# Optimization experiments

Hardware: AMD Instinct MI355X
Metric: run time of the kernel (lower is better)

Reference implementation:

```python
import jax, jax.numpy as jnp
import numpy as np
from jax.scipy.linalg import solve_triangular

L_SUB = 16          # subarray length (init arg L)
DL = 0.05           # diagonal loading factor


def setup_inputs() -> dict:
    key = jax.random.key(0)
    k0, k1, k2 = jax.random.split(key, 3)
    B, C, NS, NZ, NX = 2, 128, 1024, 256, 128
    rf = jax.random.normal(k0, (B, C, NS), jnp.float32)
    t0 = jnp.zeros((B,), jnp.float32)
    d_tx = jax.random.uniform(k1, (B, NZ, NX), dtype=jnp.float32)
    d_rx = jax.random.uniform(k2, (C, NZ, NX), dtype=jnp.float32)
    fs = jnp.float32((NS - 1) / 2.0)   # keeps sample positions in [0, NS-1]
    f0 = jnp.float32(5.0)              # unused by forward (kept for signature parity)
    c0 = jnp.float32(1.0)
    apod = jnp.ones((C,), jnp.float32) # unused by forward
    return dict(rf=rf, t0=t0, d_tx=d_tx, d_rx=d_rx, fs=fs, f0=f0, c0=c0, apod=apod)


def _aligned_signals(rf, t0, d_tx, d_rx, fs, c0):
    """Bilinear (1-D linear) resample of rf at per-pixel delays.
    Equivalent to torch grid_sample(mode='bilinear', padding_mode='border',
    align_corners=True) where the grid x-coord is samples*2/(NS-1)-1."""
    B, C, NS = rf.shape
    _, NZ, NX = d_tx.shape
    # samples: [B, C, NZ, NX] fractional sample index into rf
    samples = fs * ((d_tx[:, None, :, :] + d_rx[None, :, :, :]) / c0
                    + t0[:, None, None, None])
    pos = jnp.clip(samples, 0.0, NS - 1.0)          # border padding
    i0 = jnp.floor(pos).astype(jnp.int32)
    i1 = jnp.minimum(i0 + 1, NS - 1)
    frac = pos - i0.astype(pos.dtype)
    sig = rf.reshape(B * C, NS)
    i0f = i0.reshape(B * C, NZ * NX)
    i1f = i1.reshape(B * C, NZ * NX)
    v0 = jnp.take_along_axis(sig, i0f, axis=1).reshape(B, C, NZ, NX)
    v1 = jnp.take_along_axis(sig, i1f, axis=1).reshape(B, C, NZ, NX)
    return v0 * (1.0 - frac) + v1 * frac


def reference(rf, t0, d_tx, d_rx, fs, f0, c0, apod):
    B, C, NS = rf.shape
    _, NZ, NX = d_tx.shape
    M = C - L_SUB + 1  # number of subarrays (113)
    aligned = _aligned_signals(rf, t0, d_tx, d_rx, fs, c0)  # [B, C, NZ, NX]
    # per-pixel channel vectors: [P, C], P = B*NZ*NX
    xf = aligned.transpose(0, 2, 3, 1).reshape(-1, C)
    # subarray gather: S[p, m, l] = xf[p, m + l]  -> [P, M, L]
    idx = jnp.arange(M)[:, None] + jnp.arange(L_SUB)[None, :]
    S = xf[:, idx]
    # avg_pool1d(kernel=M, stride=1) over channels == mean over subarray axis
    x = S.mean(axis=1)                                  # [P, L]
    # spatially-smoothed covariance: R = S^T S / M, symmetrized
    R = jnp.einsum('pml,pmk->plk', S, S) / M
    R = 0.5 * (R + R.transpose(0, 2, 1))
    # diagonal loading: R += dl * (trace/L) * I
    delta = jnp.trace(R, axis1=-2, axis2=-1) / L_SUB    # [P]
    R = R + (DL * delta)[:, None, None] * jnp.eye(L_SUB, dtype=R.dtype)
    # Cholesky solve R u = 1
    Lc = jnp.linalg.cholesky(R)
    rhs = jnp.ones((R.shape[0], L_SUB, 1), R.dtype)
    y1 = solve_triangular(Lc, rhs, lower=True)
    u = solve_triangular(Lc, y1, lower=True, trans=1)[..., 0]  # [P, L]
    # MVDR weights (steering a = ones) and beamformed output
    denom = jnp.sum(u, axis=-1, keepdims=True) + 1e-10
    w = u / denom
    y = jnp.sum(w * x, axis=-1)                         # [P]
    return y.reshape(B, NZ, NX)
```

## Files before the change

kernel.cpp:

```cpp
#include <hip/hip_runtime.h>


namespace {

constexpr int kB  = 2;
constexpr int kC  = 128;
constexpr int kNS = 1024;
constexpr int kNZ = 256;
constexpr int kNX = 128;
constexpr int kZX = kNZ * kNX;
constexpr int kTPB = 256;

__device__ __host__ constexpr int tri(int l, int k) {
  return l * 16 - (l * (l - 1)) / 2 + (k - l);
}

template <bool HEAD>
__device__ __forceinline__ void chunk16(
    const float* __restrict__ rfq,
    const float* __restrict__ drxp, int cbase, float kk, float base,
    float (&F)[16], float (&win)[16], float (&head)[16], float& Sall) {
  float dr[16];
#pragma unroll
  for (int r = 0; r < 16; ++r) dr[r] = drxp[(size_t)(cbase + r) * kZX];

  float2 vv[16];
  float fr[16];
#pragma unroll
  for (int r = 0; r < 16; ++r) {
    float pos = fmaf(kk, dr[r], base);
    pos = fminf(fmaxf(pos, 0.0f), 1023.0f);
    int i0 = (int)pos;
    i0 = min(i0, kNS - 2);
    fr[r] = pos - (float)i0;
    __builtin_memcpy(&vv[r], rfq + r * kNS + i0, 8);
  }

#pragma unroll
  for (int r = 0; r < 16; ++r) {
    float v = fmaf(fr[r], vv[r].y - vv[r].x, vv[r].x);
    Sall += v;
    F[0] = fmaf(v, v, F[0]);
    if constexpr (HEAD) {
#pragma unroll
      for (int d = 1; d <= r; ++d) F[d] = fmaf(v, win[r - d], F[d]);
      head[r] = v;
    } else {
#pragma unroll
      for (int d = 1; d < 16; ++d) F[d] = fmaf(v, win[(r - d) & 15], F[d]);
    }
    win[r] = v;
  }
}

__global__ __launch_bounds__(kTPB, 1) void mvb_kernel(
    const float* __restrict__ rf, const float* __restrict__ t0,
    const float* __restrict__ d_tx, const float* __restrict__ d_rx,
    const float* __restrict__ fs_p, const float* __restrict__ c0_p,
    float* __restrict__ out) {
  const int tid = threadIdx.x;
  const int b = blockIdx.x >> 7;
  const int z = ((blockIdx.x & 127) << 1) + (tid >> 7);
  const int x = tid & 127;
  const int pix = (int)((size_t)b * kZX + z * kNX + x);

  const float fs = fs_p[0];
  const float c0 = c0_p[0];
  const float kk = fs / c0;
  const float base = fs * (d_tx[pix] / c0 + t0[b]);

  const float* rfb = rf + (size_t)b * kC * kNS;
  const float* drxp = d_rx + (size_t)z * kNX + x;

  float F[16], win[16], head[16];
  float Sall = 0.0f;
#pragma unroll
  for (int i = 0; i < 16; ++i) F[i] = 0.0f;

  chunk16<true>(rfb, drxp, 0, kk, base, F, win, head, Sall);
#pragma unroll 1
  for (int q = 1; q < 8; ++q)
    chunk16<false>(rfb + (size_t)q * 16 * kNS, drxp, q * 16, kk, base, F, win,
                   head, Sall);

  float Ru[136];
#pragma unroll
  for (int d = 0; d < 16; ++d) {
    float t0s = 0.0f;
#pragma unroll
    for (int i = d + 1; i < 16; ++i) t0s = fmaf(win[i - d], win[i], t0s);
    Ru[tri(0, d)] = F[d] - t0s;
#pragma unroll
    for (int l = 1; l < 16 - d; ++l)
      Ru[tri(l, l + d)] = Ru[tri(l - 1, l - 1 + d)] -
                          head[l - 1] * head[l - 1 + d] +
                          win[l] * win[l + d];
  }

  float tr = 0.0f;
#pragma unroll
  for (int l = 0; l < 16; ++l) tr += Ru[tri(l, l)];
  const float dl = tr * (0.05f / 16.0f);
#pragma unroll
  for (int l = 0; l < 16; ++l) Ru[tri(l, l)] += dl;

  float X[16];
  {
    float s = Sall;
#pragma unroll
    for (int i = 1; i < 16; ++i) s -= win[i];
    X[0] = s;
#pragma unroll
    for (int l = 1; l < 16; ++l) X[l] = X[l - 1] - head[l - 1] + win[l];
  }

  float inv[16];
#pragma unroll
  for (int j = 0; j < 16; ++j) {
    float d = Ru[tri(j, j)];
#pragma unroll
    for (int p = 0; p < j; ++p) d = fmaf(-Ru[tri(p, j)], Ru[tri(p, j)], d);
    inv[j] = rsqrtf(d);
#pragma unroll
    for (int i = j + 1; i < 16; ++i) {
      float s = Ru[tri(j, i)];
#pragma unroll
      for (int p = 0; p < j; ++p) s = fmaf(-Ru[tri(p, i)], Ru[tri(p, j)], s);
      Ru[tri(j, i)] = s * inv[j];
    }
  }

  float yv[16];
#pragma unroll
  for (int i = 0; i < 16; ++i) {
    float s = 1.0f;
#pragma unroll
    for (int j = 0; j < i; ++j) s = fmaf(-Ru[tri(j, i)], yv[j], s);
    yv[i] = s * inv[i];
  }
  float u[16];
#pragma unroll
  for (int i = 15; i >= 0; --i) {
    float s = yv[i];
#pragma unroll
    for (int j = i + 1; j < 16; ++j) s = fmaf(-Ru[tri(i, j)], u[j], s);
    u[i] = s * inv[i];
  }

  float su = 0.0f, dot = 0.0f;
#pragma unroll
  for (int i = 0; i < 16; ++i) {
    su += u[i];
    dot = fmaf(u[i], X[i], dot);
  }
  out[pix] = dot / (113.0f * su + 1e-10f);
}

}

extern "C" void kernel_launch(void* const* d_in, const int* in_sizes, int n_in,
                              void* d_out, int out_size, void* d_ws,
                              size_t ws_size, hipStream_t stream) {
  const float* rf   = (const float*)d_in[0];
  const float* t0   = (const float*)d_in[1];
  const float* d_tx = (const float*)d_in[2];
  const float* d_rx = (const float*)d_in[3];
  const float* fs   = (const float*)d_in[4];
  const float* c0   = (const float*)d_in[6];
  float* out = (float*)d_out;

  hipLaunchKernelGGL(mvb_kernel, dim3(kB * kNZ / 2), dim3(kTPB), 0, stream,
                     rf, t0, d_tx, d_rx, fs, c0, out);
}
```

Baseline: 95.90 us.

## Stage rf channel rows into LDS with double-buffered async global-to-LDS loads

The per-pixel gathers from rf in global memory are replaced by staging 8 channel rows (32 KB) at a time into shared memory with global_load_lds, double-buffered so the next chunk loads while the current one is gathered from LDS. The d_rx delays are also prefetched one chunk ahead in registers. The aim is to cut scattered global/L2 latency on the gathers and overlap loading with compute. In exchange it adds 64 KB of LDS per block and a barrier per chunk, and the buffer reuse depends on the async LDS writes being complete at each __syncthreads.

```diff
diff --git a/kernel.cpp b/kernel.cpp
--- a/kernel.cpp
+++ b/kernel.cpp
@@ -15,41 +15,55 @@
   return l * 16 - (l * (l - 1)) / 2 + (k - l);
 }
 
-template <bool HEAD>
-__device__ __forceinline__ void chunk16(
-    const float* __restrict__ rfq,
-    const float* __restrict__ drxp, int cbase, float kk, float base,
+__device__ __forceinline__ void stage8(const float* __restrict__ src,
+                                       float* dst, int w, int lane) {
+  const int wbase = w * 1024;
+#pragma unroll
+  for (int s = 0; s < 8; ++s) {
+    const int sb = wbase + s * 4096;
+    __builtin_amdgcn_global_load_lds(
+        (const __attribute__((address_space(1))) void*)((const char*)src + sb +
+                                                        lane * 16),
+        (__attribute__((address_space(3))) void*)((char*)dst + sb), 16, 0, 0);
+  }
+}
+
+template <int Q16, bool HEAD>
+__device__ __forceinline__ void gather8(
+    const float* __restrict__ buf, const float (&dr)[8], float kk, float base,
     float (&F)[16], float (&win)[16], float (&head)[16], float& Sall) {
-  float dr[16];
-#pragma unroll
-  for (int r = 0; r < 16; ++r) dr[r] = drxp[(size_t)(cbase + r) * kZX];
-
-  float2 vv[16];
-  float fr[16];
-#pragma unroll
-  for (int r = 0; r < 16; ++r) {
+  float fr[8];
+  int ix[8];
+#pragma unroll
+  for (int r = 0; r < 8; ++r) {
     float pos = fmaf(kk, dr[r], base);
     pos = fminf(fmaxf(pos, 0.0f), 1023.0f);
     int i0 = (int)pos;
     i0 = min(i0, kNS - 2);
     fr[r] = pos - (float)i0;
-    __builtin_memcpy(&vv[r], rfq + r * kNS + i0, 8);
-  }
-
-#pragma unroll
-  for (int r = 0; r < 16; ++r) {
-    float v = fmaf(fr[r], vv[r].y - vv[r].x, vv[r].x);
+    ix[r] = r * 1024 + i0;
+  }
+  float v0[8], v1[8];
+#pragma unroll
+  for (int r = 0; r < 8; ++r) {
+    v0[r] = buf[ix[r]];
+    v1[r] = buf[ix[r] + 1];
+  }
+#pragma unroll
+  for (int r = 0; r < 8; ++r) {
+    const int c = Q16 + r;
+    float v = fmaf(fr[r], v1[r] - v0[r], v0[r]);
     Sall += v;
     F[0] = fmaf(v, v, F[0]);
     if constexpr (HEAD) {
 #pragma unroll
-      for (int d = 1; d <= r; ++d) F[d] = fmaf(v, win[r - d], F[d]);
-      head[r] = v;
+      for (int d = 1; d <= c; ++d) F[d] = fmaf(v, win[c - d], F[d]);
+      head[c] = v;
     } else {
 #pragma unroll
-      for (int d = 1; d < 16; ++d) F[d] = fmaf(v, win[(r - d) & 15], F[d]);
-    }
-    win[r] = v;
+      for (int d = 1; d < 16; ++d) F[d] = fmaf(v, win[(c - d) & 15], F[d]);
+    }
+    win[c] = v;
   }
 }
 
@@ -58,7 +72,10 @@
     const float* __restrict__ d_tx, const float* __restrict__ d_rx,
     const float* __restrict__ fs_p, const float* __restrict__ c0_p,
     float* __restrict__ out) {
+  __shared__ float lds[2][8 * 1024];
+
   const int tid = threadIdx.x;
+  const int w = tid >> 6, lane = tid & 63;
   const int b = blockIdx.x >> 7;
   const int z = ((blockIdx.x & 127) << 1) + (tid >> 7);
   const int x = tid & 127;
@@ -77,11 +94,53 @@
 #pragma unroll
   for (int i = 0; i < 16; ++i) F[i] = 0.0f;
 
-  chunk16<true>(rfb, drxp, 0, kk, base, F, win, head, Sall);
+  float dr[8], drn[8];
+
+  stage8(rfb, lds[0], w, lane);
+#pragma unroll
+  for (int r = 0; r < 8; ++r) dr[r] = drxp[(size_t)r * kZX];
+  __syncthreads();
+
+  stage8(rfb + 8 * kNS, lds[1], w, lane);
+#pragma unroll
+  for (int r = 0; r < 8; ++r) drn[r] = drxp[(size_t)(8 + r) * kZX];
+  gather8<0, true>(lds[0], dr, kk, base, F, win, head, Sall);
+  __syncthreads();
+#pragma unroll
+  for (int r = 0; r < 8; ++r) dr[r] = drn[r];
+
+  stage8(rfb + 16 * kNS, lds[0], w, lane);
+#pragma unroll
+  for (int r = 0; r < 8; ++r) drn[r] = drxp[(size_t)(16 + r) * kZX];
+  gather8<8, true>(lds[1], dr, kk, base, F, win, head, Sall);
+  __syncthreads();
+#pragma unroll
+  for (int r = 0; r < 8; ++r) dr[r] = drn[r];
+
 #pragma unroll 1
-  for (int q = 1; q < 8; ++q)
-    chunk16<false>(rfb + (size_t)q * 16 * kNS, drxp, q * 16, kk, base, F, win,
-                   head, Sall);
+  for (int qp = 1; qp < 8; ++qp) {
+    stage8(rfb + (size_t)(2 * qp + 1) * 8 * kNS, lds[1], w, lane);
+#pragma unroll
+    for (int r = 0; r < 8; ++r)
+      drn[r] = drxp[(size_t)((2 * qp + 1) * 8 + r) * kZX];
+    gather8<0, false>(lds[0], dr, kk, base, F, win, head, Sall);
+    __syncthreads();
+#pragma unroll
+    for (int r = 0; r < 8; ++r) dr[r] = drn[r];
+
+    if (qp < 7) {
+      stage8(rfb + (size_t)(2 * qp + 2) * 8 * kNS, lds[0], w, lane);
+#pragma unroll
+      for (int r = 0; r < 8; ++r)
+        drn[r] = drxp[(size_t)((2 * qp + 2) * 8 + r) * kZX];
+    }
+    gather8<8, false>(lds[1], dr, kk, base, F, win, head, Sall);
+    if (qp < 7) {
+      __syncthreads();
+#pragma unroll
+      for (int r = 0; r < 8; ++r) dr[r] = drn[r];
+    }
+  }
 
   float Ru[136];
 #pragma unroll
```

Result: no change. 95.44 us (-0.5%).
